# Kernel optimization log

Measured on AMD Instinct MI355X. Metric: run time of the kernel, lower is better.

The kernel has to match this reference:

```python
import jax, jax.numpy as jnp
import numpy as np

B = 32; D = 192; DEPTH = 4; DI = 384; DS = 16; DC = 4; P = 16; IMG = 224; N = 196; NC = 2


def setup_inputs() -> dict:
    key = jax.random.key(0)
    ks = iter(jax.random.split(key, 20))
    rn = lambda shape, s=0.02: jax.random.normal(next(ks), shape, dtype=jnp.float32) * s
    inp = {}
    inp["x"] = jax.random.normal(next(ks), (B, 3, IMG, IMG), dtype=jnp.float32)
    inp["patch_w"] = rn((D, 3 * P * P)); inp["patch_b"] = jnp.zeros((D,), jnp.float32)
    inp["cls_token"] = rn((1, 1, D)); inp["pos_embed"] = rn((1, N + 1, D))
    inp["ln_g"] = jnp.ones((DEPTH, D), jnp.float32); inp["ln_b"] = jnp.zeros((DEPTH, D), jnp.float32)
    inp["w_in"] = rn((DEPTH, 2 * DI, D))
    inp["conv_w"] = rn((DEPTH, DI, DC)); inp["conv_b"] = jnp.zeros((DEPTH, DI), jnp.float32)
    inp["w_x"] = rn((DEPTH, 2 * DS + 1, DI))
    inp["w_dt"] = rn((DEPTH, DI)); inp["b_dt"] = jnp.zeros((DEPTH, DI), jnp.float32)
    A = jnp.tile(jnp.arange(1, DS + 1, dtype=jnp.float32)[None, None, :], (DEPTH, DI, 1))
    inp["A_log"] = jnp.log(A)
    inp["D_ssm"] = jnp.ones((DEPTH, DI), jnp.float32)
    inp["w_out"] = rn((DEPTH, D, DI))
    inp["fn_g"] = jnp.ones((D,), jnp.float32); inp["fn_b"] = jnp.zeros((D,), jnp.float32)
    inp["cls_w"] = rn((NC, D)); inp["cls_b"] = jnp.zeros((NC,), jnp.float32)
    inp["reg_w1"] = rn((D // 2, D)); inp["reg_b1"] = jnp.zeros((D // 2,), jnp.float32)
    inp["reg_w2"] = rn((1, D // 2)); inp["reg_b2"] = jnp.zeros((1,), jnp.float32)
    return inp


def _ln(x, g, b):
    m = x.mean(-1, keepdims=True)
    v = ((x - m) ** 2).mean(-1, keepdims=True)
    return (x - m) / jnp.sqrt(v + 1e-5) * g + b


def _mamba(x, w_in, conv_w, conv_b, w_x, w_dt, b_dt, A_log, D_ssm, w_out):
    Bb, L, _ = x.shape
    xz = jnp.einsum('bld,ed->ble', x, w_in)           # [B,L,2*DI]
    xc, z = xz[..., :DI], xz[..., DI:]
    # causal depthwise conv1d (torch pads both sides then slices [:L] -> left-pad DC-1)
    xct = jnp.transpose(xc, (0, 2, 1))                 # [B,DI,L]
    xpad = jnp.pad(xct, ((0, 0), (0, 0), (DC - 1, 0)))
    conv = sum(conv_w[:, k, None] * xpad[:, :, k:k + L] for k in range(DC)) + conv_b[:, None]
    xa = jax.nn.silu(jnp.transpose(conv, (0, 2, 1)))   # [B,L,DI]
    bcd = jnp.einsum('bld,nd->bln', xa, w_x)           # [B,L,2*DS+1]
    Bm = bcd[..., :DS]; Cm = bcd[..., DS:2 * DS]
    dt = jax.nn.softplus(bcd[..., -1:] * w_dt + b_dt)  # [B,L,DI]  (Linear(1,DI))
    A = -jnp.exp(A_log)                                # [DI,DS]
    dA = jnp.exp(dt[..., None] * A)                    # [B,L,DI,DS]
    dBx = dt[..., None] * Bm[:, :, None, :] * xa[..., None]

    def step(h, inp):
        dA_t, dBx_t, C_t = inp
        h = dA_t * h + dBx_t
        return h, jnp.einsum('bdn,bn->bd', h, C_t)

    h0 = jnp.zeros((Bb, DI, DS), dtype=x.dtype)
    _, ys = jax.lax.scan(step, h0, (dA.transpose(1, 0, 2, 3), dBx.transpose(1, 0, 2, 3), Cm.transpose(1, 0, 2)))
    y = jnp.transpose(ys, (1, 0, 2)) + xa * D_ssm
    return jnp.einsum('bli,di->bld', y * jax.nn.silu(z), w_out)


def reference(x, patch_w, patch_b, cls_token, pos_embed, ln_g, ln_b, w_in, conv_w, conv_b,
              w_x, w_dt, b_dt, A_log, D_ssm, w_out, fn_g, fn_b, cls_w, cls_b,
              reg_w1, reg_b1, reg_w2, reg_b2):
    Bb = x.shape[0]
    H = IMG // P
    # non-overlapping patchify == Conv2d(kernel=stride=P)
    patches = x.reshape(Bb, 3, H, P, H, P).transpose(0, 2, 4, 1, 3, 5).reshape(Bb, N, 3 * P * P)
    tok = patches @ patch_w.T + patch_b
    t = jnp.concatenate([jnp.broadcast_to(cls_token, (Bb, 1, D)), tok], axis=1) + pos_embed
    for i in range(DEPTH):
        t = t + _mamba(_ln(t, ln_g[i], ln_b[i]), w_in[i], conv_w[i], conv_b[i],
                       w_x[i], w_dt[i], b_dt[i], A_log[i], D_ssm[i], w_out[i])
    feat = _ln(t, fn_g, fn_b)[:, 0]
    cls = feat @ cls_w.T + cls_b
    reg = jax.nn.gelu(feat @ reg_w1.T + reg_b1, approximate=False) @ reg_w2.T + reg_b2
    return (cls, reg)
```

## Files before the change

### kernel.cpp

```cpp
#include <hip/hip_runtime.h>
#include <hip/hip_bf16.h>
#include <math.h>

#define B_ 32
#define D_ 192
#define DEPTH_ 4
#define DI_ 384
#define DS_ 16
#define DC_ 4
#define P_ 16
#define IMG_ 224
#define N_ 196
#define L_ 197

#define NCH 16
#define CHL 13

typedef short s16x8 __attribute__((ext_vector_type(8)));
typedef float f32x16 __attribute__((ext_vector_type(16)));

__device__ __forceinline__ float sigmoidf_(float x) { return 1.f / (1.f + expf(-x)); }

__global__ __launch_bounds__(256) void k_prep(const float* __restrict__ patch_w,
                                              const float* __restrict__ w_in,
                                              const float* __restrict__ w_out,
                                              const float* __restrict__ w_x,
                                              const float* __restrict__ cls_tok,
                                              const float* __restrict__ pos,
                                              const float* __restrict__ A_log,
                                              __hip_bfloat16* __restrict__ pw,
                                              __hip_bfloat16* __restrict__ win,
                                              __hip_bfloat16* __restrict__ wout,
                                              __hip_bfloat16* __restrict__ wx,
                                              float* __restrict__ t,
                                              float* __restrict__ Aneg) {
  int idx = blockIdx.x * 256 + threadIdx.x;
  if (idx < 147456) { pw[idx] = __float2bfloat16(patch_w[idx]); return; }
  idx -= 147456;
  if (idx < 589824) { win[idx] = __float2bfloat16(w_in[idx]); return; }
  idx -= 589824;
  if (idx < 294912) { wout[idx] = __float2bfloat16(w_out[idx]); return; }
  idx -= 294912;
  if (idx < 98304) {
    int li = idx / 24576;
    int r = (idx / 384) & 63;
    int c = idx % 384;
    wx[idx] = (r < 33) ? __float2bfloat16(w_x[(li * 33 + r) * 384 + c]) : __float2bfloat16(0.f);
    return;
  }
  idx -= 98304;
  if (idx < 6144) {
    int b = idx / 192, d = idx % 192;
    t[(size_t)b * L_ * D_ + d] = cls_tok[d] + pos[d];
    return;
  }
  idx -= 6144;
  Aneg[idx] = -expf(A_log[idx]);
}

__global__ __launch_bounds__(256) void k_im2col(const float* __restrict__ x,
                                                __hip_bfloat16* __restrict__ A) {
  int idx = blockIdx.x * 256 + threadIdx.x;
  int tok = idx / 768, f = idx - tok * 768;
  int b = tok / 196, p = tok - b * 196;
  int h = p / 14, w = p - h * 14;
  int c = f >> 8, i = (f >> 4) & 15, j = f & 15;
  float v = x[(((size_t)(b * 3 + c) * 224 + h * 16 + i) * 224 + w * 16 + j)];
  A[idx] = __float2bfloat16(v);
}

template <int KTOT, int MODE>
__global__ __launch_bounds__(256) void k_gemm_mfma(const short* __restrict__ A,
                                                   const short* __restrict__ Wb,
                                                   float* __restrict__ C,
                                                   const float* __restrict__ bias,
                                                   const float* __restrict__ pos,
                                                   int M) {
  constexpr int KC = 96;
  constexpr int STR = 104;
  __shared__ __align__(16) short Als[64 * STR];
  __shared__ __align__(16) short Bls[64 * STR];
  int m0 = blockIdx.x * 64, n0 = blockIdx.y * 64;
  int tid = threadIdx.x;
  int lane = tid & 63, wid = tid >> 6;
  int mw = (wid & 1) * 32, nw = (wid >> 1) * 32;
  int l31 = lane & 31, lh = lane >> 5;
  f32x16 acc;
#pragma unroll
  for (int i = 0; i < 16; i++) acc[i] = 0.f;
  for (int kc = 0; kc < KTOT; kc += KC) {
    __syncthreads();
#pragma unroll
    for (int i = 0; i < 3; i++) {
      int seg = tid + i * 256;
      int r = seg / 12, s = seg - r * 12;
      *(s16x8*)(Als + r * STR + s * 8) =
          *(const s16x8*)(A + (size_t)(m0 + r) * KTOT + kc + s * 8);
      *(s16x8*)(Bls + r * STR + s * 8) =
          *(const s16x8*)(Wb + (size_t)(n0 + r) * KTOT + kc + s * 8);
    }
    __syncthreads();
#pragma unroll
    for (int ks = 0; ks < KC / 16; ks++) {
      s16x8 af = *(const s16x8*)(Als + (mw + l31) * STR + ks * 16 + lh * 8);
      s16x8 bf = *(const s16x8*)(Bls + (nw + l31) * STR + ks * 16 + lh * 8);
      acc = __builtin_amdgcn_mfma_f32_32x32x16_bf16(af, bf, acc, 0, 0, 0);
    }
  }
  int gn = n0 + nw + l31;
#pragma unroll
  for (int i = 0; i < 16; i++) {
    int rowt = mw + (i & 3) + 8 * (i >> 2) + 4 * lh;
    int gm = m0 + rowt;
    float v = acc[i];
    if (MODE == 1) {
      if (gm < M) C[(size_t)gm * 192 + gn] += v;
    } else if (MODE == 3) {
      if (gm < M) C[(size_t)gm * 64 + gn] = v;
    } else if (MODE == 4) {
      if (gm < M) ((__hip_bfloat16*)C)[(size_t)gm * 768 + gn] = __float2bfloat16(v);
    } else {
      int b = gm / 196, p = gm - b * 196;
      C[((size_t)b * 197 + 1 + p) * 192 + gn] =
          v + bias[gn] + pos[(size_t)(1 + p) * 192 + gn];
    }
  }
}

__global__ __launch_bounds__(256) void k_ln_bf(const float* __restrict__ t,
                                               const float* __restrict__ g,
                                               const float* __restrict__ bb,
                                               __hip_bfloat16* __restrict__ o) {
  int tok = blockIdx.x * 4 + (threadIdx.x >> 6);
  int tid = threadIdx.x & 63;
  const float* xr = t + (size_t)tok * D_;
  float x0 = xr[tid], x1 = xr[tid + 64], x2 = xr[tid + 128];
  float s = x0 + x1 + x2;
  float q = x0 * x0 + x1 * x1 + x2 * x2;
#pragma unroll
  for (int off = 1; off < 64; off <<= 1) {
    s += __shfl_xor(s, off, 64);
    q += __shfl_xor(q, off, 64);
  }
  float m = s * (1.f / 192.f);
  float r = rsqrtf(q * (1.f / 192.f) - m * m + 1e-5f);
  __hip_bfloat16* orow = o + (size_t)tok * D_;
  orow[tid]       = __float2bfloat16((x0 - m) * r * g[tid]       + bb[tid]);
  orow[tid + 64]  = __float2bfloat16((x1 - m) * r * g[tid + 64]  + bb[tid + 64]);
  orow[tid + 128] = __float2bfloat16((x2 - m) * r * g[tid + 128] + bb[tid + 128]);
}

__global__ __launch_bounds__(384) void k_conv(const __hip_bfloat16* __restrict__ xz,
                                              const float* __restrict__ cw_,
                                              const float* __restrict__ cb,
                                              __hip_bfloat16* __restrict__ xa_bf,
                                              __hip_bfloat16* __restrict__ sz_bf) {
  __shared__ float xs[11][384];
  int r0 = blockIdx.x * 8;
  int d = threadIdx.x;
#pragma unroll
  for (int row = 0; row < 11; row++) {
    int gr = r0 - 3 + row;
    if (gr >= 0) xs[row][d] = __bfloat162float(xz[(size_t)gr * 768 + d]);
  }
  __syncthreads();
  float4 cw = *(const float4*)(cw_ + d * 4);
  float cbv = cb[d];
#pragma unroll
  for (int tk = 0; tk < 8; tk++) {
    int tok = r0 + tk;
    int l = tok % L_;
    float acc = fmaf(cw.w, xs[tk + 3][d], cbv);
    if (l >= 1) acc = fmaf(cw.z, xs[tk + 2][d], acc);
    if (l >= 2) acc = fmaf(cw.y, xs[tk + 1][d], acc);
    if (l >= 3) acc = fmaf(cw.x, xs[tk][d], acc);
    float xav = acc * sigmoidf_(acc);
    xa_bf[(size_t)tok * DI_ + d] = __float2bfloat16(xav);
    float z = __bfloat162float(xz[(size_t)tok * 768 + 384 + d]);
    sz_bf[(size_t)tok * DI_ + d] = __float2bfloat16(z * sigmoidf_(z));
  }
}

__global__ __launch_bounds__(384) void k_scan1(const __hip_bfloat16* __restrict__ xa,
                                               const float* __restrict__ bcd,
                                               const float* __restrict__ Aneg,
                                               const float* __restrict__ w_dt,
                                               const float* __restrict__ b_dt,
                                               float* __restrict__ Pst,
                                               float* __restrict__ Hst) {
  int b = blockIdx.x >> 4, ch = blockIdx.x & 15;
  int d = threadIdx.x;
  int l0 = ch * CHL;
  int lim = min(CHL, L_ - l0);
  float Av[16];
#pragma unroll
  for (int q = 0; q < 4; q++) {
    float4 v = *(const float4*)(Aneg + d * 16 + q * 4);
    Av[q * 4] = v.x; Av[q * 4 + 1] = v.y; Av[q * 4 + 2] = v.z; Av[q * 4 + 3] = v.w;
  }
  float wdt = w_dt[d], bdt = b_dt[d];
  const __hip_bfloat16* xap = xa + ((size_t)b * L_ + l0) * DI_ + d;
  const float* bp = bcd + ((size_t)b * L_ + l0) * 64;
  float h[16], Pp[16];
#pragma unroll
  for (int n = 0; n < 16; n++) { h[n] = 0.f; Pp[n] = 1.f; }
  float xv = __bfloat162float(xap[0]);
  for (int j = 0; j < lim; j++) {
    int jn = (j + 1 < lim) ? (j + 1) : j;
    float xn = __bfloat162float(xap[(size_t)jn * DI_]);
    float dtraw = bp[j * 64 + 32];
    float Bn[16];
#pragma unroll
    for (int n = 0; n < 16; n++) Bn[n] = bp[j * 64 + n];
    float v = fmaf(dtraw, wdt, bdt);
    float dtv = (v > 20.f) ? v : __logf(1.f + __expf(v));
    float dtx = dtv * xv;
#pragma unroll
    for (int n = 0; n < 16; n++) {
      float dA = __expf(dtv * Av[n]);
      h[n] = fmaf(dA, h[n], dtx * Bn[n]);
      Pp[n] *= dA;
    }
    xv = xn;
  }
  size_t s = ((size_t)blockIdx.x * 384 + d) * 16;
#pragma unroll
  for (int q = 0; q < 4; q++) {
    *(float4*)(Pst + s + q * 4) = make_float4(Pp[q * 4], Pp[q * 4 + 1], Pp[q * 4 + 2], Pp[q * 4 + 3]);
    *(float4*)(Hst + s + q * 4) = make_float4(h[q * 4], h[q * 4 + 1], h[q * 4 + 2], h[q * 4 + 3]);
  }
}

__global__ __launch_bounds__(256) void k_scan_mid(const float* __restrict__ Pst,
                                                  const float* __restrict__ Hst,
                                                  float* __restrict__ Hinit) {
  int idx = blockIdx.x * 256 + threadIdx.x;
  int b = idx / 6144, r = idx - b * 6144;
  float h = 0.f;
#pragma unroll
  for (int c = 0; c < NCH; c++) {
    size_t o = (size_t)(b * NCH + c) * 6144 + r;
    Hinit[o] = h;
    h = fmaf(Pst[o], h, Hst[o]);
  }
}

__global__ __launch_bounds__(384) void k_scan2(const __hip_bfloat16* __restrict__ xa,
                                               const __hip_bfloat16* __restrict__ sz,
                                               const float* __restrict__ bcd,
                                               const float* __restrict__ Aneg,
                                               const float* __restrict__ D_ssm,
                                               const float* __restrict__ w_dt,
                                               const float* __restrict__ b_dt,
                                               const float* __restrict__ Hinit,
                                               __hip_bfloat16* __restrict__ y) {
  int b = blockIdx.x >> 4, ch = blockIdx.x & 15;
  int d = threadIdx.x;
  int l0 = ch * CHL;
  int lim = min(CHL, L_ - l0);
  float Av[16];
#pragma unroll
  for (int q = 0; q < 4; q++) {
    float4 v = *(const float4*)(Aneg + d * 16 + q * 4);
    Av[q * 4] = v.x; Av[q * 4 + 1] = v.y; Av[q * 4 + 2] = v.z; Av[q * 4 + 3] = v.w;
  }
  float Dv = D_ssm[d];
  float wdt = w_dt[d], bdt = b_dt[d];
  const __hip_bfloat16* xap = xa + ((size_t)b * L_ + l0) * DI_ + d;
  const __hip_bfloat16* szp = sz + ((size_t)b * L_ + l0) * DI_ + d;
  const float* bp = bcd + ((size_t)b * L_ + l0) * 64;
  __hip_bfloat16* yp = y + ((size_t)b * L_ + l0) * DI_ + d;
  float h[16];
  {
    size_t s = ((size_t)blockIdx.x * 384 + d) * 16;
#pragma unroll
    for (int q = 0; q < 4; q++) {
      float4 v = *(const float4*)(Hinit + s + q * 4);
      h[q * 4] = v.x; h[q * 4 + 1] = v.y; h[q * 4 + 2] = v.z; h[q * 4 + 3] = v.w;
    }
  }
  float xv = __bfloat162float(xap[0]);
  float szv = __bfloat162float(szp[0]);
  for (int j = 0; j < lim; j++) {
    int jn = (j + 1 < lim) ? (j + 1) : j;
    float xn = __bfloat162float(xap[(size_t)jn * DI_]);
    float szn = __bfloat162float(szp[(size_t)jn * DI_]);
    float dtraw = bp[j * 64 + 32];
    float Bn[16], Cn[16];
#pragma unroll
    for (int n = 0; n < 16; n++) Bn[n] = bp[j * 64 + n];
#pragma unroll
    for (int n = 0; n < 16; n++) Cn[n] = bp[j * 64 + 16 + n];
    float v = fmaf(dtraw, wdt, bdt);
    float dtv = (v > 20.f) ? v : __logf(1.f + __expf(v));
    float dtx = dtv * xv;
    float acc = 0.f;
#pragma unroll
    for (int n = 0; n < 16; n++) {
      float dA = __expf(dtv * Av[n]);
      h[n] = fmaf(dA, h[n], dtx * Bn[n]);
      acc = fmaf(h[n], Cn[n], acc);
    }
    float yv = fmaf(xv, Dv, acc) * szv;
    yp[(size_t)j * DI_] = __float2bfloat16(yv);
    xv = xn; szv = szn;
  }
}

__global__ __launch_bounds__(192) void k_head(const float* __restrict__ t,
                                              const float* __restrict__ fn_g,
                                              const float* __restrict__ fn_b,
                                              const float* __restrict__ cls_w,
                                              const float* __restrict__ cls_b,
                                              const float* __restrict__ rw1,
                                              const float* __restrict__ rb1,
                                              const float* __restrict__ rw2,
                                              const float* __restrict__ rb2,
                                              float* __restrict__ out) {
  __shared__ float red[8];
  __shared__ float stats[2];
  __shared__ float feat_s[192];
  __shared__ float h_s[96];
  int b = blockIdx.x, tid = threadIdx.x;
  float x = t[(size_t)b * L_ * D_ + tid];
  float s = x, q = x * x;
#pragma unroll
  for (int off = 1; off < 64; off <<= 1) {
    s += __shfl_xor(s, off, 64);
    q += __shfl_xor(q, off, 64);
  }
  int w = tid >> 6;
  if ((tid & 63) == 0) { red[w] = s; red[4 + w] = q; }
  __syncthreads();
  if (tid == 0) {
    float ss = red[0] + red[1] + red[2];
    float qq = red[4] + red[5] + red[6];
    float m = ss * (1.f / 192.f);
    stats[0] = m;
    stats[1] = rsqrtf(qq * (1.f / 192.f) - m * m + 1e-5f);
  }
  __syncthreads();
  float fv = (x - stats[0]) * stats[1] * fn_g[tid] + fn_b[tid];
  feat_s[tid] = fv;
  __syncthreads();
  if (tid < 96) {
    float a = rb1[tid];
    const float* wr = rw1 + (size_t)tid * 192;
    for (int k = 0; k < 192; k++) a = fmaf(feat_s[k], wr[k], a);
    h_s[tid] = 0.5f * a * (1.f + erff(a * 0.70710678118654752f));
  } else if (tid < 98) {
    int c = tid - 96;
    float a = cls_b[c];
    const float* wr = cls_w + (size_t)c * 192;
    for (int k = 0; k < 192; k++) a = fmaf(feat_s[k], wr[k], a);
    out[b * 2 + c] = a;
  }
  __syncthreads();
  if (tid == 0) {
    float a = rb2[0];
    for (int j = 0; j < 96; j++) a = fmaf(h_s[j], rw2[j], a);
    out[64 + b] = a;
  }
}

extern "C" void kernel_launch(void* const* d_in, const int* in_sizes, int n_in,
                              void* d_out, int out_size, void* d_ws, size_t ws_size,
                              hipStream_t stream) {
  const float* x       = (const float*)d_in[0];
  const float* patch_w = (const float*)d_in[1];
  const float* patch_b = (const float*)d_in[2];
  const float* cls_tok = (const float*)d_in[3];
  const float* pos     = (const float*)d_in[4];
  const float* ln_g    = (const float*)d_in[5];
  const float* ln_b    = (const float*)d_in[6];
  const float* w_in    = (const float*)d_in[7];
  const float* conv_w  = (const float*)d_in[8];
  const float* conv_b  = (const float*)d_in[9];
  const float* w_x     = (const float*)d_in[10];
  const float* w_dt    = (const float*)d_in[11];
  const float* b_dt    = (const float*)d_in[12];
  const float* A_log   = (const float*)d_in[13];
  const float* D_ssm   = (const float*)d_in[14];
  const float* w_out   = (const float*)d_in[15];
  const float* fn_g    = (const float*)d_in[16];
  const float* fn_b    = (const float*)d_in[17];
  const float* cls_w   = (const float*)d_in[18];
  const float* cls_b   = (const float*)d_in[19];
  const float* reg_w1  = (const float*)d_in[20];
  const float* reg_b1  = (const float*)d_in[21];
  const float* reg_w2  = (const float*)d_in[22];
  const float* reg_b2  = (const float*)d_in[23];
  float* out = (float*)d_out;

  float* ws = (float*)d_ws;
  float* t_buf = ws;
  float* bcd   = t_buf + 1210368;
  float* Pst   = bcd + 405504;
  float* Hst   = Pst + 3145728;
  float* Hinit = Hst + 3145728;
  float* Aneg  = Hinit + 3145728;
  __hip_bfloat16* xz_bf  = (__hip_bfloat16*)(Aneg + 24576);
  __hip_bfloat16* Abuf   = xz_bf;
  __hip_bfloat16* xa_bf  = xz_bf + 4841472;
  __hip_bfloat16* sz_bf  = xa_bf + 2433024;
  __hip_bfloat16* xln_bf = sz_bf + 2433024;
  __hip_bfloat16* y_bf   = xln_bf + 1216512;
  __hip_bfloat16* pw_bf  = y_bf + 2433024;
  __hip_bfloat16* win_bf = pw_bf + 147456;
  __hip_bfloat16* wout_bf = win_bf + 589824;
  __hip_bfloat16* wx_bf  = wout_bf + 294912;

  k_prep<<<4536, 256, 0, stream>>>(patch_w, w_in, w_out, w_x, cls_tok, pos, A_log,
                                   pw_bf, win_bf, wout_bf, wx_bf, t_buf, Aneg);
  k_im2col<<<18816, 256, 0, stream>>>(x, Abuf);
  k_gemm_mfma<768, 2><<<dim3(98, 3), 256, 0, stream>>>(
      (const short*)Abuf, (const short*)pw_bf, t_buf, patch_b, pos, 6272);

  for (int i = 0; i < DEPTH_; i++) {
    k_ln_bf<<<1576, 256, 0, stream>>>(t_buf, ln_g + i * D_, ln_b + i * D_, xln_bf);
    k_gemm_mfma<192, 4><<<dim3(99, 12), 256, 0, stream>>>(
        (const short*)xln_bf, (const short*)(win_bf + (size_t)i * 147456), (float*)xz_bf,
        nullptr, nullptr, 6304);
    k_conv<<<788, 384, 0, stream>>>(xz_bf, conv_w + i * DI_ * DC_, conv_b + i * DI_,
                                    xa_bf, sz_bf);
    k_gemm_mfma<384, 3><<<dim3(99, 1), 256, 0, stream>>>(
        (const short*)xa_bf, (const short*)(wx_bf + (size_t)i * 24576), bcd,
        nullptr, nullptr, 6304);
    k_scan1<<<B_ * NCH, 384, 0, stream>>>(xa_bf, bcd, Aneg + i * 6144,
                                          w_dt + i * DI_, b_dt + i * DI_, Pst, Hst);
    k_scan_mid<<<768, 256, 0, stream>>>(Pst, Hst, Hinit);
    k_scan2<<<B_ * NCH, 384, 0, stream>>>(xa_bf, sz_bf, bcd, Aneg + i * 6144,
                                          D_ssm + i * DI_, w_dt + i * DI_, b_dt + i * DI_,
                                          Hinit, y_bf);
    k_gemm_mfma<384, 1><<<dim3(99, 3), 256, 0, stream>>>(
        (const short*)y_bf, (const short*)(wout_bf + (size_t)i * 73728), t_buf,
        nullptr, nullptr, 6304);
  }
  k_head<<<32, 192, 0, stream>>>(t_buf, fn_g, fn_b, cls_w, cls_b, reg_w1, reg_b1,
                                 reg_w2, reg_b2, out);
}
```

Baseline: 467.9 us.

## Fuse LayerNorm into in-projection GEMM and x-projection GEMM into conv kernel

LayerNorm is computed inside the in-projection GEMM prologue: each block normalizes its 64 rows and writes the bf16 result straight into shared memory. This removes the separate LN kernel and its bf16 round trip through global memory. The small x-projection GEMM (bcd) now runs inside the conv kernel on the 16 freshly computed xa rows held in shared memory, removing another launch and a global reread. The generic GEMM K-chunk is also doubled to 192, which raises shared memory use and redundantly recomputes LN statistics for every column-block of the in-projection GEMM.

```diff
diff --git a/kernel.cpp b/kernel.cpp
--- a/kernel.cpp
+++ b/kernel.cpp
@@ -20,6 +20,10 @@
 typedef float f32x16 __attribute__((ext_vector_type(16)));
 
 __device__ __forceinline__ float sigmoidf_(float x) { return 1.f / (1.f + expf(-x)); }
+__device__ __forceinline__ short f2bf(float x) {
+  __hip_bfloat16 h = __float2bfloat16(x);
+  return *reinterpret_cast<short*>(&h);
+}
 
 __global__ __launch_bounds__(256) void k_prep(const float* __restrict__ patch_w,
                                               const float* __restrict__ w_in,
@@ -76,8 +80,8 @@
                                                    const float* __restrict__ bias,
                                                    const float* __restrict__ pos,
                                                    int M) {
-  constexpr int KC = 96;
-  constexpr int STR = 104;
+  constexpr int KC = 192;
+  constexpr int STR = 200;
   __shared__ __align__(16) short Als[64 * STR];
   __shared__ __align__(16) short Bls[64 * STR];
   int m0 = blockIdx.x * 64, n0 = blockIdx.y * 64;
@@ -91,9 +95,9 @@
   for (int kc = 0; kc < KTOT; kc += KC) {
     __syncthreads();
 #pragma unroll
-    for (int i = 0; i < 3; i++) {
+    for (int i = 0; i < KC / 32; i++) {
       int seg = tid + i * 256;
-      int r = seg / 12, s = seg - r * 12;
+      int r = seg / 24, s = seg - r * 24;
       *(s16x8*)(Als + r * STR + s * 8) =
           *(const s16x8*)(A + (size_t)(m0 + r) * KTOT + kc + s * 8);
       *(s16x8*)(Bls + r * STR + s * 8) =
@@ -115,10 +119,6 @@
     float v = acc[i];
     if (MODE == 1) {
       if (gm < M) C[(size_t)gm * 192 + gn] += v;
-    } else if (MODE == 3) {
-      if (gm < M) C[(size_t)gm * 64 + gn] = v;
-    } else if (MODE == 4) {
-      if (gm < M) ((__hip_bfloat16*)C)[(size_t)gm * 768 + gn] = __float2bfloat16(v);
     } else {
       int b = gm / 196, p = gm - b * 196;
       C[((size_t)b * 197 + 1 + p) * 192 + gn] =
@@ -127,39 +127,119 @@
   }
 }
 
-__global__ __launch_bounds__(256) void k_ln_bf(const float* __restrict__ t,
-                                               const float* __restrict__ g,
-                                               const float* __restrict__ bb,
-                                               __hip_bfloat16* __restrict__ o) {
-  int tok = blockIdx.x * 4 + (threadIdx.x >> 6);
-  int tid = threadIdx.x & 63;
-  const float* xr = t + (size_t)tok * D_;
-  float x0 = xr[tid], x1 = xr[tid + 64], x2 = xr[tid + 128];
-  float s = x0 + x1 + x2;
-  float q = x0 * x0 + x1 * x1 + x2 * x2;
-#pragma unroll
-  for (int off = 1; off < 64; off <<= 1) {
-    s += __shfl_xor(s, off, 64);
-    q += __shfl_xor(q, off, 64);
-  }
-  float m = s * (1.f / 192.f);
-  float r = rsqrtf(q * (1.f / 192.f) - m * m + 1e-5f);
-  __hip_bfloat16* orow = o + (size_t)tok * D_;
-  orow[tid]       = __float2bfloat16((x0 - m) * r * g[tid]       + bb[tid]);
-  orow[tid + 64]  = __float2bfloat16((x1 - m) * r * g[tid + 64]  + bb[tid + 64]);
-  orow[tid + 128] = __float2bfloat16((x2 - m) * r * g[tid + 128] + bb[tid + 128]);
-}
-
-__global__ __launch_bounds__(384) void k_conv(const __hip_bfloat16* __restrict__ xz,
-                                              const float* __restrict__ cw_,
-                                              const float* __restrict__ cb,
-                                              __hip_bfloat16* __restrict__ xa_bf,
-                                              __hip_bfloat16* __restrict__ sz_bf) {
-  __shared__ float xs[11][384];
-  int r0 = blockIdx.x * 8;
+__global__ __launch_bounds__(256) void k_gemm_ln(const float* __restrict__ t,
+                                                 const float* __restrict__ g,
+                                                 const float* __restrict__ bvec,
+                                                 const short* __restrict__ Wb,
+                                                 __hip_bfloat16* __restrict__ xz,
+                                                 int M) {
+  constexpr int STR = 200;
+  __shared__ __align__(16) short Als[64 * STR];
+  __shared__ __align__(16) short Bls[64 * STR];
+  int m0 = blockIdx.x * 64, n0 = blockIdx.y * 64;
+  int tid = threadIdx.x;
+  {
+    int r = tid >> 2, q = tid & 3;
+    const float* row = t + (size_t)(m0 + r) * 192 + q * 48;
+    float4 v0 = *(const float4*)(row + 0);
+    float4 v1 = *(const float4*)(row + 4);
+    float4 v2 = *(const float4*)(row + 8);
+    float4 v3 = *(const float4*)(row + 12);
+    float4 v4 = *(const float4*)(row + 16);
+    float4 v5 = *(const float4*)(row + 20);
+    float4 v6 = *(const float4*)(row + 24);
+    float4 v7 = *(const float4*)(row + 28);
+    float4 v8 = *(const float4*)(row + 32);
+    float4 v9 = *(const float4*)(row + 36);
+    float4 va = *(const float4*)(row + 40);
+    float4 vb = *(const float4*)(row + 44);
+    float s = v0.x + v0.y + v0.z + v0.w + v1.x + v1.y + v1.z + v1.w +
+              v2.x + v2.y + v2.z + v2.w + v3.x + v3.y + v3.z + v3.w +
+              v4.x + v4.y + v4.z + v4.w + v5.x + v5.y + v5.z + v5.w +
+              v6.x + v6.y + v6.z + v6.w + v7.x + v7.y + v7.z + v7.w +
+              v8.x + v8.y + v8.z + v8.w + v9.x + v9.y + v9.z + v9.w +
+              va.x + va.y + va.z + va.w + vb.x + vb.y + vb.z + vb.w;
+    float qs = v0.x*v0.x + v0.y*v0.y + v0.z*v0.z + v0.w*v0.w +
+               v1.x*v1.x + v1.y*v1.y + v1.z*v1.z + v1.w*v1.w +
+               v2.x*v2.x + v2.y*v2.y + v2.z*v2.z + v2.w*v2.w +
+               v3.x*v3.x + v3.y*v3.y + v3.z*v3.z + v3.w*v3.w +
+               v4.x*v4.x + v4.y*v4.y + v4.z*v4.z + v4.w*v4.w +
+               v5.x*v5.x + v5.y*v5.y + v5.z*v5.z + v5.w*v5.w +
+               v6.x*v6.x + v6.y*v6.y + v6.z*v6.z + v6.w*v6.w +
+               v7.x*v7.x + v7.y*v7.y + v7.z*v7.z + v7.w*v7.w +
+               v8.x*v8.x + v8.y*v8.y + v8.z*v8.z + v8.w*v8.w +
+               v9.x*v9.x + v9.y*v9.y + v9.z*v9.z + v9.w*v9.w +
+               va.x*va.x + va.y*va.y + va.z*va.z + va.w*va.w +
+               vb.x*vb.x + vb.y*vb.y + vb.z*vb.z + vb.w*vb.w;
+    s += __shfl_xor(s, 1, 64);  s += __shfl_xor(s, 2, 64);
+    qs += __shfl_xor(qs, 1, 64); qs += __shfl_xor(qs, 2, 64);
+    float m = s * (1.f / 192.f);
+    float rstd = rsqrtf(qs * (1.f / 192.f) - m * m + 1e-5f);
+    short* arow = Als + r * STR + q * 48;
+    const float* gq = g + q * 48;
+    const float* bq = bvec + q * 48;
+    float4 vv[12] = {v0, v1, v2, v3, v4, v5, v6, v7, v8, v9, va, vb};
+#pragma unroll
+    for (int k2 = 0; k2 < 6; k2++) {
+      float4 x0 = vv[2 * k2], x1 = vv[2 * k2 + 1];
+      float4 g0 = *(const float4*)(gq + k2 * 8);
+      float4 g1 = *(const float4*)(gq + k2 * 8 + 4);
+      float4 b0 = *(const float4*)(bq + k2 * 8);
+      float4 b1 = *(const float4*)(bq + k2 * 8 + 4);
+      s16x8 o;
+      o[0] = f2bf((x0.x - m) * rstd * g0.x + b0.x);
+      o[1] = f2bf((x0.y - m) * rstd * g0.y + b0.y);
+      o[2] = f2bf((x0.z - m) * rstd * g0.z + b0.z);
+      o[3] = f2bf((x0.w - m) * rstd * g0.w + b0.w);
+      o[4] = f2bf((x1.x - m) * rstd * g1.x + b1.x);
+      o[5] = f2bf((x1.y - m) * rstd * g1.y + b1.y);
+      o[6] = f2bf((x1.z - m) * rstd * g1.z + b1.z);
+      o[7] = f2bf((x1.w - m) * rstd * g1.w + b1.w);
+      *(s16x8*)(arow + k2 * 8) = o;
+    }
+  }
+#pragma unroll
+  for (int i = 0; i < 6; i++) {
+    int seg = tid + i * 256;
+    int r = seg / 24, sc = seg - r * 24;
+    *(s16x8*)(Bls + r * STR + sc * 8) =
+        *(const s16x8*)(Wb + (size_t)(n0 + r) * 192 + sc * 8);
+  }
+  __syncthreads();
+  int lane = tid & 63, wid = tid >> 6;
+  int mw = (wid & 1) * 32, nw = (wid >> 1) * 32;
+  int l31 = lane & 31, lh = lane >> 5;
+  f32x16 acc;
+#pragma unroll
+  for (int i = 0; i < 16; i++) acc[i] = 0.f;
+#pragma unroll
+  for (int ks = 0; ks < 12; ks++) {
+    s16x8 af = *(const s16x8*)(Als + (mw + l31) * STR + ks * 16 + lh * 8);
+    s16x8 bf = *(const s16x8*)(Bls + (nw + l31) * STR + ks * 16 + lh * 8);
+    acc = __builtin_amdgcn_mfma_f32_32x32x16_bf16(af, bf, acc, 0, 0, 0);
+  }
+  int gn = n0 + nw + l31;
+#pragma unroll
+  for (int i = 0; i < 16; i++) {
+    int rowt = mw + (i & 3) + 8 * (i >> 2) + 4 * lh;
+    int gm = m0 + rowt;
+    if (gm < M) xz[(size_t)gm * 768 + gn] = __float2bfloat16(acc[i]);
+  }
+}
+
+__global__ __launch_bounds__(384) void k_conv_bcd(const __hip_bfloat16* __restrict__ xz,
+                                                  const float* __restrict__ cw_,
+                                                  const float* __restrict__ cb,
+                                                  const short* __restrict__ wx,
+                                                  __hip_bfloat16* __restrict__ xa_bf,
+                                                  __hip_bfloat16* __restrict__ sz_bf,
+                                                  float* __restrict__ bcd) {
+  __shared__ float xs[19][384];
+  __shared__ __align__(16) short xa_s[16 * 392];
+  int r0 = blockIdx.x * 16;
   int d = threadIdx.x;
 #pragma unroll
-  for (int row = 0; row < 11; row++) {
+  for (int row = 0; row < 19; row++) {
     int gr = r0 - 3 + row;
     if (gr >= 0) xs[row][d] = __bfloat162float(xz[(size_t)gr * 768 + d]);
   }
@@ -167,7 +247,7 @@
   float4 cw = *(const float4*)(cw_ + d * 4);
   float cbv = cb[d];
 #pragma unroll
-  for (int tk = 0; tk < 8; tk++) {
+  for (int tk = 0; tk < 16; tk++) {
     int tok = r0 + tk;
     int l = tok % L_;
     float acc = fmaf(cw.w, xs[tk + 3][d], cbv);
@@ -175,9 +255,34 @@
     if (l >= 2) acc = fmaf(cw.y, xs[tk + 1][d], acc);
     if (l >= 3) acc = fmaf(cw.x, xs[tk][d], acc);
     float xav = acc * sigmoidf_(acc);
-    xa_bf[(size_t)tok * DI_ + d] = __float2bfloat16(xav);
+    short hv = f2bf(xav);
+    xa_bf[(size_t)tok * DI_ + d] = *reinterpret_cast<__hip_bfloat16*>(&hv);
+    xa_s[tk * 392 + d] = hv;
     float z = __bfloat162float(xz[(size_t)tok * 768 + 384 + d]);
     sz_bf[(size_t)tok * DI_ + d] = __float2bfloat16(z * sigmoidf_(z));
+  }
+  __syncthreads();
+  int wid = d >> 6;
+  if (wid < 2) {
+    int lane = d & 63, l31 = lane & 31, lh = lane >> 5;
+    int n0w = wid * 32;
+    f32x16 acc;
+#pragma unroll
+    for (int i = 0; i < 16; i++) acc[i] = 0.f;
+    const short* wrow = wx + (size_t)(n0w + l31) * 384;
+    const s16x8 zf = {0, 0, 0, 0, 0, 0, 0, 0};
+#pragma unroll
+    for (int ks = 0; ks < 24; ks++) {
+      s16x8 af = *(const s16x8*)(xa_s + (l31 & 15) * 392 + ks * 16 + lh * 8);
+      if (l31 >= 16) af = zf;
+      s16x8 bf = *(const s16x8*)(wrow + ks * 16 + lh * 8);
+      acc = __builtin_amdgcn_mfma_f32_32x32x16_bf16(af, bf, acc, 0, 0, 0);
+    }
+#pragma unroll
+    for (int i = 0; i < 16; i++) {
+      int rowt = (i & 3) + 8 * (i >> 2) + 4 * lh;
+      if (rowt < 16) bcd[(size_t)(r0 + rowt) * 64 + n0w + l31] = acc[i];
+    }
   }
 }
 
@@ -417,15 +522,12 @@
       (const short*)Abuf, (const short*)pw_bf, t_buf, patch_b, pos, 6272);
 
   for (int i = 0; i < DEPTH_; i++) {
-    k_ln_bf<<<1576, 256, 0, stream>>>(t_buf, ln_g + i * D_, ln_b + i * D_, xln_bf);
-    k_gemm_mfma<192, 4><<<dim3(99, 12), 256, 0, stream>>>(
-        (const short*)xln_bf, (const short*)(win_bf + (size_t)i * 147456), (float*)xz_bf,
-        nullptr, nullptr, 6304);
-    k_conv<<<788, 384, 0, stream>>>(xz_bf, conv_w + i * DI_ * DC_, conv_b + i * DI_,
-                                    xa_bf, sz_bf);
-    k_gemm_mfma<384, 3><<<dim3(99, 1), 256, 0, stream>>>(
-        (const short*)xa_bf, (const short*)(wx_bf + (size_t)i * 24576), bcd,
-        nullptr, nullptr, 6304);
+    k_gemm_ln<<<dim3(99, 12), 256, 0, stream>>>(
+        t_buf, ln_g + i * D_, ln_b + i * D_,
+        (const short*)(win_bf + (size_t)i * 147456), xz_bf, 6304);
+    k_conv_bcd<<<394, 384, 0, stream>>>(xz_bf, conv_w + i * DI_ * DC_, conv_b + i * DI_,
+                                        (const short*)(wx_bf + (size_t)i * 24576),
+                                        xa_bf, sz_bf, bcd);
     k_scan1<<<B_ * NCH, 384, 0, stream>>>(xa_bf, bcd, Aneg + i * 6144,
                                           w_dt + i * DI_, b_dt + i * DI_, Pst, Hst);
     k_scan_mid<<<768, 256, 0, stream>>>(Pst, Hst, Hinit);
```

Result: slower. 500.6 us (+7.0%).
